# Kernel tuning notes

Hardware: AMD Instinct MI355X
Metric: run time of the kernel (lower is better)

The kernel has to match this reference:

```python
import jax, jax.numpy as jnp
import numpy as np

B, N, D = 4, 1024, 1024
NH = 16
HS = D // NH
HID = 4 * D
EPS = 1e-5

def layernorm(x, w, b):
    mu = jnp.mean(x, axis=-1, keepdims=True)
    var = jnp.mean(jnp.square(x - mu), axis=-1, keepdims=True)
    return (x - mu) * jax.lax.rsqrt(var + EPS) * w + b

def setup_inputs() -> dict:
    key = jax.random.key(0)
    ks = jax.random.split(key, 8)
    s = lambda fan_in: 1.0 / np.sqrt(fan_in)
    return {
        "x": jax.random.normal(ks[0], (B, N, D), jnp.float32),
        "qkv_w": jax.random.uniform(ks[1], (3 * D, D), jnp.float32, -s(D), s(D)),
        "proj_w": jax.random.uniform(ks[2], (D, D), jnp.float32, -s(D), s(D)),
        "proj_b": jax.random.uniform(ks[3], (D,), jnp.float32, -s(D), s(D)),
        "ln1_w": jnp.ones((D,), jnp.float32),
        "ln1_b": jnp.zeros((D,), jnp.float32),
        "fc1_w": jax.random.uniform(ks[4], (HID, D), jnp.float32, -s(D), s(D)),
        "fc1_b": jax.random.uniform(ks[5], (HID,), jnp.float32, -s(D), s(D)),
        "fc2_w": jax.random.uniform(ks[6], (D, HID), jnp.float32, -s(HID), s(HID)),
        "fc2_b": jax.random.uniform(ks[7], (D,), jnp.float32, -s(HID), s(HID)),
        "ln2_w": jnp.ones((D,), jnp.float32),
        "ln2_b": jnp.zeros((D,), jnp.float32),
    }

def attention(x, qkv_w, proj_w, proj_b):
    # x: [b, n, d]; qkv linear (no bias), split into q,k,v per head
    qkv = jnp.einsum('bnd,ed->bne', x, qkv_w)              # [b, n, 3d]
    qkv = qkv.reshape(B, N, 3, NH, HS).transpose(2, 0, 3, 1, 4)  # [3, b, nh, n, hs]
    q, k, v = qkv[0], qkv[1], qkv[2]
    scale = HS ** -0.5
    # mask=False => self.mask == 1, so (mask-1)*LARGE_NUMBER == 0
    att = jax.nn.softmax(scale * jnp.einsum('bhqe,bhke->bhqk', q, k), axis=-1)
    y = jnp.einsum('bhqk,bhke->bhqe', att, v)              # [b, nh, n, hs]
    y = y.transpose(0, 2, 1, 3).reshape(B, N, D)
    return jnp.einsum('bnd,ed->bne', y, proj_w) + proj_b

def mlp(x, fc1_w, fc1_b, fc2_w, fc2_b):
    h = jax.nn.gelu(jnp.einsum('bnd,hd->bnh', x, fc1_w) + fc1_b, approximate=False)
    return jnp.einsum('bnh,dh->bnd', h, fc2_w) + fc2_b

def reference(x, qkv_w, proj_w, proj_b, ln1_w, ln1_b, fc1_w, fc1_b, fc2_w, fc2_b, ln2_w, ln2_b):
    x = x + attention(layernorm(x, ln1_w, ln1_b), qkv_w, proj_w, proj_b)
    x = x + mlp(layernorm(x, ln2_w, ln2_b), fc1_w, fc1_b, fc2_w, fc2_b)
    return x
```

## Files before the change

### kernel.cpp

```cpp
#include <hip/hip_runtime.h>
#include <hip/hip_bf16.h>

typedef __attribute__((ext_vector_type(8))) short short8;
typedef __attribute__((ext_vector_type(8))) unsigned short ushort8;
typedef __attribute__((ext_vector_type(4))) float floatx4;

#define DEV static __device__ __forceinline__

DEV unsigned short f2bf(float f) {
  unsigned int u = __builtin_bit_cast(unsigned int, f);
  u += 0x7fff + ((u >> 16) & 1);
  return (unsigned short)(u >> 16);
}
DEV float bf2f(unsigned short u) {
  return __builtin_bit_cast(float, (unsigned int)u << 16);
}

DEV void gload_lds16(const void* g, void* l) {
  __builtin_amdgcn_global_load_lds(
      (const __attribute__((address_space(1))) unsigned int*)g,
      (__attribute__((address_space(3))) unsigned int*)l, 16, 0, 0);
}

__global__ __launch_bounds__(256) void cvt4_kernel(const float* __restrict__ w0,
                                                   const float* __restrict__ w1,
                                                   const float* __restrict__ w2,
                                                   const float* __restrict__ w3,
                                                   unsigned short* __restrict__ o0,
                                                   unsigned short* __restrict__ o1,
                                                   unsigned short* __restrict__ o2,
                                                   unsigned short* __restrict__ o3) {
  int i = blockIdx.x * 256 + threadIdx.x;
  const float* in; unsigned short* out; int j;
  if (i < 786432)       { in = w0; out = o0; j = i; }
  else if (i < 1048576) { in = w1; out = o1; j = i - 786432; }
  else if (i < 2097152) { in = w2; out = o2; j = i - 1048576; }
  else                  { in = w3; out = o3; j = i - 2097152; }
  float4 v = reinterpret_cast<const float4*>(in)[j];
  ushort4 o;
  o.x = f2bf(v.x); o.y = f2bf(v.y); o.z = f2bf(v.z); o.w = f2bf(v.w);
  reinterpret_cast<ushort4*>(out)[j] = o;
}

__global__ __launch_bounds__(256) void ln_kernel(const float* __restrict__ x,
                                                 const float* __restrict__ w,
                                                 const float* __restrict__ b,
                                                 unsigned short* __restrict__ out) {
  const int row = blockIdx.x;
  const float* xr = x + (size_t)row * 1024;
  float4 v = reinterpret_cast<const float4*>(xr)[threadIdx.x];
  float s  = v.x + v.y + v.z + v.w;
  float ss = v.x*v.x + v.y*v.y + v.z*v.z + v.w*v.w;
  #pragma unroll
  for (int off = 1; off < 64; off <<= 1) {
    s  += __shfl_xor(s, off);
    ss += __shfl_xor(ss, off);
  }
  __shared__ float red[8];
  const int wid = threadIdx.x >> 6, lane = threadIdx.x & 63;
  if (lane == 0) { red[wid] = s; red[4 + wid] = ss; }
  __syncthreads();
  s  = red[0] + red[1] + red[2] + red[3];
  ss = red[4] + red[5] + red[6] + red[7];
  const float mu  = s * (1.0f / 1024.0f);
  const float var = ss * (1.0f / 1024.0f) - mu * mu;
  const float rstd = rsqrtf(var + 1e-5f);
  float4 wv = reinterpret_cast<const float4*>(w)[threadIdx.x];
  float4 bv = reinterpret_cast<const float4*>(b)[threadIdx.x];
  ushort4 o;
  o.x = f2bf((v.x - mu) * rstd * wv.x + bv.x);
  o.y = f2bf((v.y - mu) * rstd * wv.y + bv.y);
  o.z = f2bf((v.z - mu) * rstd * wv.z + bv.z);
  o.w = f2bf((v.w - mu) * rstd * wv.w + bv.w);
  reinterpret_cast<ushort4*>(out)[(size_t)row * 256 + threadIdx.x] = o;
}

template<int EPI>
__global__ __launch_bounds__(512, 2) void gemm256(const unsigned short* __restrict__ A,
                                                  const unsigned short* __restrict__ Bw,
                                                  unsigned short* __restrict__ outb,
                                                  const float* __restrict__ bias,
                                                  int K, int N, int NT) {
  __shared__ unsigned short As[2][256 * 64];
  __shared__ unsigned short Bs[2][256 * 64];
  const int tid = threadIdx.x, lane = tid & 63, wid = tid >> 6;
  const int wr = wid >> 2, wc = wid & 3;
  const int fr = lane & 15, s0 = lane >> 4;

  const int nwg = gridDim.x;
  const int qq = nwg >> 3, rr8 = nwg & 7, xcd = blockIdx.x & 7, lid = blockIdx.x >> 3;
  const int wg = (xcd < rr8 ? xcd * (qq + 1) : rr8 * (qq + 1) + (xcd - rr8) * qq) + lid;
  const int brow = (wg / NT) * 256, bcol = (wg % NT) * 256;

  const unsigned short* ag[4];
  const unsigned short* bg[4];
  #pragma unroll
  for (int L = 0; L < 4; L++) {
    const int idx = L * 512 + tid;
    const int row = idx >> 3;
    const int ss  = ((idx & 7) ^ (row & 7)) * 8;
    ag[L] = A  + (size_t)(brow + row) * K + ss;
    bg[L] = Bw + (size_t)(bcol + row) * K + ss;
  }
  const int ldst = tid * 8;

  #define STG256(kt, buf)                                                     \
    do {                                                                      \
      const int ko = (kt) * 64;                                               \
      gload_lds16(ag[0] + ko, &As[buf][ldst]);                                \
      gload_lds16(ag[1] + ko, &As[buf][4096 + ldst]);                         \
      gload_lds16(ag[2] + ko, &As[buf][8192 + ldst]);                         \
      gload_lds16(ag[3] + ko, &As[buf][12288 + ldst]);                        \
      gload_lds16(bg[0] + ko, &Bs[buf][ldst]);                                \
      gload_lds16(bg[1] + ko, &Bs[buf][4096 + ldst]);                         \
      gload_lds16(bg[2] + ko, &Bs[buf][8192 + ldst]);                         \
      gload_lds16(bg[3] + ko, &Bs[buf][12288 + ldst]);                        \
    } while (0)

  const int xs = fr & 7;
  const int aoff = (wr * 128 + fr) * 64;
  const int boff = (wc * 64 + fr) * 64;
  const int sl0 = ((0 + s0) ^ xs) * 8;
  const int sl1 = ((4 + s0) ^ xs) * 8;

  floatx4 acc[8][4];
  #pragma unroll
  for (int m = 0; m < 8; m++)
    #pragma unroll
    for (int n = 0; n < 4; n++) acc[m][n] = (floatx4){0.f, 0.f, 0.f, 0.f};

  const int NTK = K >> 6;
  STG256(0, 0);

  for (int kt = 0; kt < NTK; ++kt) {
    const int cur = kt & 1;
    if (kt + 1 < NTK) {
      STG256(kt + 1, cur ^ 1);
      asm volatile("s_waitcnt vmcnt(8)" ::: "memory");
    } else {
      asm volatile("s_waitcnt vmcnt(0)" ::: "memory");
    }
    __builtin_amdgcn_s_barrier();

    const unsigned short* Ac = As[cur];
    const unsigned short* Bc = Bs[cur];
    short8 a0[4][2], a1[4][2], b0[2][2], b1[2][2];

    #pragma unroll
    for (int m = 0; m < 4; m++) {
      a0[m][0] = *reinterpret_cast<const short8*>(Ac + aoff + m * 1024 + sl0);
      a0[m][1] = *reinterpret_cast<const short8*>(Ac + aoff + m * 1024 + sl1);
    }
    #pragma unroll
    for (int n = 0; n < 2; n++) {
      b0[n][0] = *reinterpret_cast<const short8*>(Bc + boff + n * 1024 + sl0);
      b0[n][1] = *reinterpret_cast<const short8*>(Bc + boff + n * 1024 + sl1);
    }
    __builtin_amdgcn_s_barrier();
    __builtin_amdgcn_s_setprio(1);
    #pragma unroll
    for (int m = 0; m < 4; m++)
      #pragma unroll
      for (int n = 0; n < 2; n++) {
        acc[m][n] = __builtin_amdgcn_mfma_f32_16x16x32_bf16(a0[m][0], b0[n][0], acc[m][n], 0, 0, 0);
        acc[m][n] = __builtin_amdgcn_mfma_f32_16x16x32_bf16(a0[m][1], b0[n][1], acc[m][n], 0, 0, 0);
      }
    __builtin_amdgcn_s_setprio(0);
    __builtin_amdgcn_s_barrier();

    #pragma unroll
    for (int n = 0; n < 2; n++) {
      b1[n][0] = *reinterpret_cast<const short8*>(Bc + boff + (n + 2) * 1024 + sl0);
      b1[n][1] = *reinterpret_cast<const short8*>(Bc + boff + (n + 2) * 1024 + sl1);
    }
    __builtin_amdgcn_s_barrier();
    __builtin_amdgcn_s_setprio(1);
    #pragma unroll
    for (int m = 0; m < 4; m++)
      #pragma unroll
      for (int n = 0; n < 2; n++) {
        acc[m][n + 2] = __builtin_amdgcn_mfma_f32_16x16x32_bf16(a0[m][0], b1[n][0], acc[m][n + 2], 0, 0, 0);
        acc[m][n + 2] = __builtin_amdgcn_mfma_f32_16x16x32_bf16(a0[m][1], b1[n][1], acc[m][n + 2], 0, 0, 0);
      }
    __builtin_amdgcn_s_setprio(0);
    __builtin_amdgcn_s_barrier();

    #pragma unroll
    for (int m = 0; m < 4; m++) {
      a1[m][0] = *reinterpret_cast<const short8*>(Ac + aoff + (m + 4) * 1024 + sl0);
      a1[m][1] = *reinterpret_cast<const short8*>(Ac + aoff + (m + 4) * 1024 + sl1);
    }
    __builtin_amdgcn_s_barrier();
    __builtin_amdgcn_s_setprio(1);
    #pragma unroll
    for (int m = 0; m < 4; m++)
      #pragma unroll
      for (int n = 0; n < 2; n++) {
        acc[m + 4][n] = __builtin_amdgcn_mfma_f32_16x16x32_bf16(a1[m][0], b0[n][0], acc[m + 4][n], 0, 0, 0);
        acc[m + 4][n] = __builtin_amdgcn_mfma_f32_16x16x32_bf16(a1[m][1], b0[n][1], acc[m + 4][n], 0, 0, 0);
      }
    __builtin_amdgcn_s_setprio(0);
    __builtin_amdgcn_s_barrier();

    __builtin_amdgcn_s_setprio(1);
    #pragma unroll
    for (int m = 0; m < 4; m++)
      #pragma unroll
      for (int n = 0; n < 2; n++) {
        acc[m + 4][n + 2] = __builtin_amdgcn_mfma_f32_16x16x32_bf16(a1[m][0], b1[n][0], acc[m + 4][n + 2], 0, 0, 0);
        acc[m + 4][n + 2] = __builtin_amdgcn_mfma_f32_16x16x32_bf16(a1[m][1], b1[n][1], acc[m + 4][n + 2], 0, 0, 0);
      }
    __builtin_amdgcn_s_setprio(0);
    __builtin_amdgcn_s_barrier();
  }
  #undef STG256

  #pragma unroll
  for (int m = 0; m < 8; m++) {
    #pragma unroll
    for (int n = 0; n < 4; n++) {
      const int col = bcol + wc * 64 + n * 16 + fr;
      #pragma unroll
      for (int r = 0; r < 4; r++) {
        const size_t idx = (size_t)(brow + wr * 128 + m * 16 + s0 * 4 + r) * N + col;
        float v = acc[m][n][r];
        if (EPI == 1) {
          v += bias[col];
          const float u = v * 0.7978845608f * (1.0f + 0.044715f * v * v);
          const float e = __expf(2.0f * u);
          v = v * (e / (e + 1.0f));
        }
        outb[idx] = f2bf(v);
      }
    }
  }
}

__global__ __launch_bounds__(512) void gemm128sk(const unsigned short* __restrict__ A,
                                                 const unsigned short* __restrict__ Bw,
                                                 unsigned short* __restrict__ outb,
                                                 int K, int Ksl, int N, int NT, int ntiles) {
  __shared__ unsigned short As[4][128 * 32];
  __shared__ unsigned short Bs[4][128 * 32];
  const int tid = threadIdx.x, lane = tid & 63, wid = tid >> 6;
  const int wrow = (wid >> 2) * 64, wcol = (wid & 3) * 32;
  const int fr = lane & 15, s0 = lane >> 4;

  const int nwg = gridDim.x;
  const int qq = nwg >> 3, rr8 = nwg & 7, xcd = blockIdx.x & 7, lid = blockIdx.x >> 3;
  const int wg = (xcd < rr8 ? xcd * (qq + 1) : rr8 * (qq + 1) + (xcd - rr8) * qq) + lid;
  const int kslice = wg / ntiles, t = wg % ntiles;
  const int brow = (t / NT) * 128, bcol = (t % NT) * 128;
  const int kofs = kslice * Ksl;

  const int srow = tid >> 2;
  const int sslot = ((tid & 3) ^ ((srow >> 1) & 3)) * 8;
  const unsigned short* ag = A  + (size_t)(brow + srow) * K + kofs + sslot;
  const unsigned short* bg = Bw + (size_t)(bcol + srow) * K + kofs + sslot;
  const int ldst = tid * 8;

  #define STG(kt, buf)                              \
    do {                                            \
      const int ko = (kt) * 32;                     \
      gload_lds16(ag + ko, &As[buf][ldst]);         \
      gload_lds16(bg + ko, &Bs[buf][ldst]);         \
    } while (0)

  const int slr = (s0 ^ ((fr >> 1) & 3)) * 8;

  floatx4 acc[4][2];
  #pragma unroll
  for (int i = 0; i < 4; i++)
    #pragma unroll
    for (int j = 0; j < 2; j++) acc[i][j] = (floatx4){0.f, 0.f, 0.f, 0.f};

  const int NTK = Ksl >> 5;
  STG(0, 0);
  STG(1, 1);
  STG(2, 2);

  for (int kt = 0; kt < NTK; ++kt) {
    const int cur = kt & 3;
    if (kt + 3 < NTK) {
      STG(kt + 3, (kt + 3) & 3);
      asm volatile("s_waitcnt vmcnt(6)" ::: "memory");
    } else if (kt + 2 < NTK) {
      asm volatile("s_waitcnt vmcnt(4)" ::: "memory");
    } else if (kt + 1 < NTK) {
      asm volatile("s_waitcnt vmcnt(2)" ::: "memory");
    } else {
      asm volatile("s_waitcnt vmcnt(0)" ::: "memory");
    }
    __builtin_amdgcn_s_barrier();

    short8 af[4], bf[2];
    #pragma unroll
    for (int i = 0; i < 4; i++)
      af[i] = *reinterpret_cast<const short8*>(&As[cur][(wrow + i * 16 + fr) * 32 + slr]);
    #pragma unroll
    for (int j = 0; j < 2; j++)
      bf[j] = *reinterpret_cast<const short8*>(&Bs[cur][(wcol + j * 16 + fr) * 32 + slr]);
    __builtin_amdgcn_s_setprio(1);
    #pragma unroll
    for (int i = 0; i < 4; i++)
      #pragma unroll
      for (int j = 0; j < 2; j++)
        acc[i][j] = __builtin_amdgcn_mfma_f32_16x16x32_bf16(af[i], bf[j], acc[i][j], 0, 0, 0);
    __builtin_amdgcn_s_setprio(0);
    __builtin_amdgcn_s_barrier();
  }
  #undef STG

  unsigned short* po = outb + (size_t)kslice * ((size_t)ntiles * 16384);
  const int erow = brow + wrow + (s0 << 2);
  const int ecol = bcol + wcol + fr;
  #pragma unroll
  for (int i = 0; i < 4; i++)
    #pragma unroll
    for (int j = 0; j < 2; j++)
      #pragma unroll
      for (int r = 0; r < 4; r++)
        po[(size_t)(erow + i * 16 + r) * N + ecol + j * 16] = f2bf(acc[i][j][r]);
}

__global__ __launch_bounds__(256) void red_ln(const unsigned short* __restrict__ p0,
                                              const unsigned short* __restrict__ p1,
                                              const float* __restrict__ x,
                                              const float* __restrict__ bias,
                                              const float* __restrict__ lw,
                                              const float* __restrict__ lb,
                                              float* __restrict__ x1,
                                              unsigned short* __restrict__ xn) {
  const int row = blockIdx.x, t = threadIdx.x;
  const size_t o4 = (size_t)row * 256 + t;
  ushort4 a = reinterpret_cast<const ushort4*>(p0)[o4];
  ushort4 c = reinterpret_cast<const ushort4*>(p1)[o4];
  float4 xv = reinterpret_cast<const float4*>(x)[o4];
  float4 bv = reinterpret_cast<const float4*>(bias)[t];
  float4 v;
  v.x = bf2f(a.x) + bf2f(c.x) + bv.x + xv.x;
  v.y = bf2f(a.y) + bf2f(c.y) + bv.y + xv.y;
  v.z = bf2f(a.z) + bf2f(c.z) + bv.z + xv.z;
  v.w = bf2f(a.w) + bf2f(c.w) + bv.w + xv.w;
  reinterpret_cast<float4*>(x1)[o4] = v;

  float s  = v.x + v.y + v.z + v.w;
  float ss = v.x*v.x + v.y*v.y + v.z*v.z + v.w*v.w;
  #pragma unroll
  for (int off = 1; off < 64; off <<= 1) {
    s  += __shfl_xor(s, off);
    ss += __shfl_xor(ss, off);
  }
  __shared__ float red[8];
  const int wid = t >> 6, lane = t & 63;
  if (lane == 0) { red[wid] = s; red[4 + wid] = ss; }
  __syncthreads();
  s  = red[0] + red[1] + red[2] + red[3];
  ss = red[4] + red[5] + red[6] + red[7];
  const float mu  = s * (1.0f / 1024.0f);
  const float var = ss * (1.0f / 1024.0f) - mu * mu;
  const float rstd = rsqrtf(var + 1e-5f);
  float4 wv = reinterpret_cast<const float4*>(lw)[t];
  float4 lv = reinterpret_cast<const float4*>(lb)[t];
  ushort4 o;
  o.x = f2bf((v.x - mu) * rstd * wv.x + lv.x);
  o.y = f2bf((v.y - mu) * rstd * wv.y + lv.y);
  o.z = f2bf((v.z - mu) * rstd * wv.z + lv.z);
  o.w = f2bf((v.w - mu) * rstd * wv.w + lv.w);
  reinterpret_cast<ushort4*>(xn)[o4] = o;
}

__global__ __launch_bounds__(256) void red_out(const unsigned short* __restrict__ p0,
                                               const unsigned short* __restrict__ p1,
                                               const float* __restrict__ x1,
                                               const float* __restrict__ bias,
                                               float* __restrict__ out) {
  const size_t i4 = (size_t)blockIdx.x * 256 + threadIdx.x;
  const int c4 = (int)(i4 & 255);
  ushort4 a = reinterpret_cast<const ushort4*>(p0)[i4];
  ushort4 c = reinterpret_cast<const ushort4*>(p1)[i4];
  float4 xv = reinterpret_cast<const float4*>(x1)[i4];
  float4 bv = reinterpret_cast<const float4*>(bias)[c4];
  float4 v;
  v.x = bf2f(a.x) + bf2f(c.x) + bv.x + xv.x;
  v.y = bf2f(a.y) + bf2f(c.y) + bv.y + xv.y;
  v.z = bf2f(a.z) + bf2f(c.z) + bv.z + xv.z;
  v.w = bf2f(a.w) + bf2f(c.w) + bv.w + xv.w;
  reinterpret_cast<float4*>(out)[i4] = v;
}

__global__ __launch_bounds__(256) void vtrans_kernel(const unsigned short* __restrict__ qkv,
                                                     unsigned short* __restrict__ vt) {
  __shared__ unsigned short T[64][66];
  const int nt = blockIdx.x, bh = blockIdx.y;
  const int b = bh >> 4, h = bh & 15;
  const unsigned short* src = qkv + (size_t)b * 1024 * 3072 + 2048 + h * 64;
  const int r = threadIdx.x >> 3, s = threadIdx.x & 7;
  ushort8 a0 = *reinterpret_cast<const ushort8*>(src + (size_t)(nt * 64 + r) * 3072 + s * 8);
  ushort8 a1 = *reinterpret_cast<const ushort8*>(src + (size_t)(nt * 64 + r + 32) * 3072 + s * 8);
  #pragma unroll
  for (int j = 0; j < 8; j++) {
    T[r][s * 8 + j]      = a0[j];
    T[r + 32][s * 8 + j] = a1[j];
  }
  __syncthreads();
  ushort8 o0, o1;
  #pragma unroll
  for (int j = 0; j < 8; j++) {
    o0[j] = T[s * 8 + j][r];
    o1[j] = T[s * 8 + j][r + 32];
  }
  unsigned short* dst = vt + (size_t)bh * 64 * 1024 + nt * 64 + s * 8;
  *reinterpret_cast<ushort8*>(dst + (size_t)r * 1024)        = o0;
  *reinterpret_cast<ushort8*>(dst + (size_t)(r + 32) * 1024) = o1;
}

__global__ __launch_bounds__(256) void attn_kernel(const unsigned short* __restrict__ qkv,
                                                   const unsigned short* __restrict__ vt,
                                                   unsigned short* __restrict__ y) {
  __shared__ unsigned short Ks[2][64 * 64];
  __shared__ unsigned short Vs[2][64 * 64];
  __shared__ unsigned short Ps[4][16 * 64];

  const int tid = threadIdx.x;
  const int lane = tid & 63;
  const int w = tid >> 6;
  const int wg = (blockIdx.x & 7) * 128 + (blockIdx.x >> 3);
  const int bh = wg >> 4, qt = wg & 15;
  const int b = bh >> 4, h = bh & 15;
  const int fr = lane & 15, s0 = lane >> 4;
  const int fk = s0 * 8;
  const int sw = fr & 7;
  const size_t RS = 3072;

  const unsigned short* qbase = qkv + (size_t)b * 1024 * RS + h * 64;
  const unsigned short* kbase = qbase + 1024;
  const unsigned short* vbase = vt + (size_t)bh * 64 * 1024;

  short8 aq[2];
  {
    const unsigned short* qrow = qbase + (size_t)(qt * 64 + w * 16 + fr) * RS;
    aq[0] = *reinterpret_cast<const short8*>(qrow + fk);
    aq[1] = *reinterpret_cast<const short8*>(qrow + 32 + fk);
  }

  float m_run[4], l_run[4];
  floatx4 accy[4];
  #pragma unroll
  for (int r = 0; r < 4; r++) { m_run[r] = -1e30f; l_run[r] = 0.f; }
  #pragma unroll
  for (int d = 0; d < 4; d++) accy[d] = (floatx4){0.f, 0.f, 0.f, 0.f};

  const int krow0 = tid >> 3, kslot = tid & 7;
  const int gslot = (kslot ^ (krow0 & 7)) * 8;
  const unsigned short* kg0 = kbase + (size_t)krow0 * RS + gslot;
  const unsigned short* kg1 = kbase + (size_t)(krow0 + 32) * RS + gslot;
  const unsigned short* vg0 = vbase + (size_t)krow0 * 1024 + gslot;
  const unsigned short* vg1 = vbase + (size_t)(krow0 + 32) * 1024 + gslot;

  #define STAGE(t, buf)                                          \
    do {                                                         \
      const size_t ko = (size_t)(t) * 64 * RS;                   \
      const size_t vo = (size_t)(t) * 64;                        \
      gload_lds16(kg0 + ko, &Ks[buf][tid * 8]);                  \
      gload_lds16(kg1 + ko, &Ks[buf][(256 + tid) * 8]);          \
      gload_lds16(vg0 + vo, &Vs[buf][tid * 8]);                  \
      gload_lds16(vg1 + vo, &Vs[buf][(256 + tid) * 8]);          \
    } while (0)

  STAGE(0, 0);
  int cur = 0;

  for (int kt = 0; kt < 16; ++kt) {
    if (kt < 15) {
      STAGE(kt + 1, cur ^ 1);
      asm volatile("s_waitcnt vmcnt(4)" ::: "memory");
    } else {
      asm volatile("s_waitcnt vmcnt(0)" ::: "memory");
    }
    __builtin_amdgcn_s_barrier();

    const unsigned short* Kt = Ks[cur];
    const unsigned short* Vc = Vs[cur];

    floatx4 sfr[4];
    #pragma unroll
    for (int f = 0; f < 4; ++f) {
      floatx4 s = (floatx4){0.f, 0.f, 0.f, 0.f};
      const unsigned short* krow = Kt + (f * 16 + fr) * 64;
      short8 kb0 = *reinterpret_cast<const short8*>(krow + (((s0)     ^ sw) << 3));
      short8 kb1 = *reinterpret_cast<const short8*>(krow + (((s0 + 4) ^ sw) << 3));
      s = __builtin_amdgcn_mfma_f32_16x16x32_bf16(aq[0], kb0, s, 0, 0, 0);
      s = __builtin_amdgcn_mfma_f32_16x16x32_bf16(aq[1], kb1, s, 0, 0, 0);
      sfr[f] = s * 0.125f;
    }

    #pragma unroll
    for (int r = 0; r < 4; r++) {
      float mv = fmaxf(fmaxf(sfr[0][r], sfr[1][r]), fmaxf(sfr[2][r], sfr[3][r]));
      #pragma unroll
      for (int m = 1; m < 16; m <<= 1) mv = fmaxf(mv, __shfl_xor(mv, m));
      const float mn = fmaxf(m_run[r], mv);
      const float alpha = __expf(m_run[r] - mn);
      m_run[r] = mn;
      const int q = s0 * 4 + r;
      const int qx = (q & 7) << 3;
      float ps = 0.f;
      #pragma unroll
      for (int f = 0; f < 4; f++) {
        float p = __expf(sfr[f][r] - mn);
        ps += p;
        Ps[w][q * 64 + ((f * 16 + fr) ^ qx)] = f2bf(p);
      }
      #pragma unroll
      for (int m = 1; m < 16; m <<= 1) ps += __shfl_xor(ps, m);
      l_run[r] = l_run[r] * alpha + ps;
      #pragma unroll
      for (int d = 0; d < 4; d++) accy[d][r] *= alpha;
    }

    #pragma unroll
    for (int ks = 0; ks < 2; ++ks) {
      const int sA = ((ks * 4 + s0) ^ sw) << 3;
      short8 ap = *reinterpret_cast<const short8*>(&Ps[w][fr * 64 + sA]);
      #pragma unroll
      for (int j = 0; j < 4; ++j) {
        short8 vb = *reinterpret_cast<const short8*>(Vc + (j * 16 + fr) * 64 + sA);
        accy[j] = __builtin_amdgcn_mfma_f32_16x16x32_bf16(ap, vb, accy[j], 0, 0, 0);
      }
    }
    __builtin_amdgcn_s_barrier();
    cur ^= 1;
  }
  #undef STAGE

  #pragma unroll
  for (int r = 0; r < 4; r++) {
    const float inv = 1.0f / l_run[r];
    const size_t grow =
        (size_t)(b * 1024 + qt * 64 + w * 16 + s0 * 4 + r) * 1024 + h * 64;
    #pragma unroll
    for (int d = 0; d < 4; ++d)
      y[grow + d * 16 + fr] = f2bf(accy[d][r] * inv);
  }
}

extern "C" void kernel_launch(void* const* d_in, const int* in_sizes, int n_in,
                              void* d_out, int out_size, void* d_ws, size_t ws_size,
                              hipStream_t stream) {
  const float* x      = (const float*)d_in[0];
  const float* qkv_w  = (const float*)d_in[1];
  const float* proj_w = (const float*)d_in[2];
  const float* proj_b = (const float*)d_in[3];
  const float* ln1_w  = (const float*)d_in[4];
  const float* ln1_b  = (const float*)d_in[5];
  const float* fc1_w  = (const float*)d_in[6];
  const float* fc1_b  = (const float*)d_in[7];
  const float* fc2_w  = (const float*)d_in[8];
  const float* fc2_b  = (const float*)d_in[9];
  const float* ln2_w  = (const float*)d_in[10];
  const float* ln2_b  = (const float*)d_in[11];
  float* out = (float*)d_out;

  char* ws = (char*)d_ws;
  unsigned short* qkvw16  = (unsigned short*)(ws + 0);
  unsigned short* projw16 = (unsigned short*)(ws + 6291456);
  unsigned short* fc1w16  = (unsigned short*)(ws + 8388608);
  unsigned short* fc2w16  = (unsigned short*)(ws + 16777216);
  float*          x1      = (float*)(ws + 25165824);
  unsigned short* vt      = (unsigned short*)(ws + 25165824);
  unsigned short* xn      = (unsigned short*)(ws + 41943040);
  unsigned short* big     = (unsigned short*)(ws + 50331648);
  unsigned short* pp      = big;
  unsigned short* fp      = (unsigned short*)(ws + 0);

  cvt4_kernel<<<12288, 256, 0, stream>>>(qkv_w, proj_w, fc1_w, fc2_w,
                                         qkvw16, projw16, fc1w16, fc2w16);

  ln_kernel<<<4096, 256, 0, stream>>>(x, ln1_w, ln1_b, xn);
  gemm256<0><<<192, 512, 0, stream>>>(xn, qkvw16, big, nullptr, 1024, 3072, 12);
  vtrans_kernel<<<dim3(16, 64), 256, 0, stream>>>(big, vt);
  attn_kernel<<<1024, 256, 0, stream>>>(big, vt, xn);
  gemm128sk<<<512, 512, 0, stream>>>(xn, projw16, pp, 1024, 512, 1024, 8, 256);
  red_ln<<<4096, 256, 0, stream>>>(pp, pp + 4194304, x, proj_b, ln2_w, ln2_b, x1, xn);
  gemm256<1><<<256, 512, 0, stream>>>(xn, fc1w16, big, fc1_b, 1024, 4096, 16);
  gemm128sk<<<512, 512, 0, stream>>>(big, fc2w16, fp, 4096, 2048, 1024, 8, 256);
  red_out<<<4096, 256, 0, stream>>>(fp, fp + 4194304, x1, fc2_b, out);
}
```

Measured before the change: 252.7 us.

## Read K/V directly from global memory in attention, add lazy rescaling and exp2 softmax

The attention kernel drops the double-buffered LDS staging of K and V tiles and its barriers. Each wave now loads K and V fragments straight from global memory, relying on the caches, and raises wave priority around the MFMA blocks. Softmax switches to exp2 with the log2e factor folded into the scale. The running max and accumulator rescale now happen only when some row's max grows by more than a threshold. This removes barriers and LDS traffic, but adds redundant global loads across the four waves and accepts bounded growth in the unnormalised accumulator.

```diff
diff --git a/kernel.cpp b/kernel.cpp
--- a/kernel.cpp
+++ b/kernel.cpp
@@ -418,8 +418,6 @@
 __global__ __launch_bounds__(256) void attn_kernel(const unsigned short* __restrict__ qkv,
                                                    const unsigned short* __restrict__ vt,
                                                    unsigned short* __restrict__ y) {
-  __shared__ unsigned short Ks[2][64 * 64];
-  __shared__ unsigned short Vs[2][64 * 64];
   __shared__ unsigned short Ps[4][16 * 64];
 
   const int tid = threadIdx.x;
@@ -429,8 +427,6 @@
   const int bh = wg >> 4, qt = wg & 15;
   const int b = bh >> 4, h = bh & 15;
   const int fr = lane & 15, s0 = lane >> 4;
-  const int fk = s0 * 8;
-  const int sw = fr & 7;
   const size_t RS = 3072;
 
   const unsigned short* qbase = qkv + (size_t)b * 1024 * RS + h * 64;
@@ -440,10 +436,11 @@
   short8 aq[2];
   {
     const unsigned short* qrow = qbase + (size_t)(qt * 64 + w * 16 + fr) * RS;
-    aq[0] = *reinterpret_cast<const short8*>(qrow + fk);
-    aq[1] = *reinterpret_cast<const short8*>(qrow + 32 + fk);
-  }
-
+    aq[0] = *reinterpret_cast<const short8*>(qrow + s0 * 8);
+    aq[1] = *reinterpret_cast<const short8*>(qrow + 32 + s0 * 8);
+  }
+
+  const float SC = 0.125f * 1.44269504089f;
   float m_run[4], l_run[4];
   floatx4 accy[4];
   #pragma unroll
@@ -451,97 +448,86 @@
   #pragma unroll
   for (int d = 0; d < 4; d++) accy[d] = (floatx4){0.f, 0.f, 0.f, 0.f};
 
-  const int krow0 = tid >> 3, kslot = tid & 7;
-  const int gslot = (kslot ^ (krow0 & 7)) * 8;
-  const unsigned short* kg0 = kbase + (size_t)krow0 * RS + gslot;
-  const unsigned short* kg1 = kbase + (size_t)(krow0 + 32) * RS + gslot;
-  const unsigned short* vg0 = vbase + (size_t)krow0 * 1024 + gslot;
-  const unsigned short* vg1 = vbase + (size_t)(krow0 + 32) * 1024 + gslot;
-
-  #define STAGE(t, buf)                                          \
-    do {                                                         \
-      const size_t ko = (size_t)(t) * 64 * RS;                   \
-      const size_t vo = (size_t)(t) * 64;                        \
-      gload_lds16(kg0 + ko, &Ks[buf][tid * 8]);                  \
-      gload_lds16(kg1 + ko, &Ks[buf][(256 + tid) * 8]);          \
-      gload_lds16(vg0 + vo, &Vs[buf][tid * 8]);                  \
-      gload_lds16(vg1 + vo, &Vs[buf][(256 + tid) * 8]);          \
-    } while (0)
-
-  STAGE(0, 0);
-  int cur = 0;
+  const int sw = fr & 7;
 
   for (int kt = 0; kt < 16; ++kt) {
-    if (kt < 15) {
-      STAGE(kt + 1, cur ^ 1);
-      asm volatile("s_waitcnt vmcnt(4)" ::: "memory");
-    } else {
-      asm volatile("s_waitcnt vmcnt(0)" ::: "memory");
-    }
-    __builtin_amdgcn_s_barrier();
-
-    const unsigned short* Kt = Ks[cur];
-    const unsigned short* Vc = Vs[cur];
+    const int kvoff = kt * 64;
 
     floatx4 sfr[4];
+    __builtin_amdgcn_s_setprio(1);
     #pragma unroll
     for (int f = 0; f < 4; ++f) {
+      const unsigned short* kg = kbase + (size_t)(kvoff + f * 16 + fr) * RS + s0 * 8;
+      short8 kb0 = *reinterpret_cast<const short8*>(kg);
+      short8 kb1 = *reinterpret_cast<const short8*>(kg + 32);
       floatx4 s = (floatx4){0.f, 0.f, 0.f, 0.f};
-      const unsigned short* krow = Kt + (f * 16 + fr) * 64;
-      short8 kb0 = *reinterpret_cast<const short8*>(krow + (((s0)     ^ sw) << 3));
-      short8 kb1 = *reinterpret_cast<const short8*>(krow + (((s0 + 4) ^ sw) << 3));
       s = __builtin_amdgcn_mfma_f32_16x16x32_bf16(aq[0], kb0, s, 0, 0, 0);
       s = __builtin_amdgcn_mfma_f32_16x16x32_bf16(aq[1], kb1, s, 0, 0, 0);
-      sfr[f] = s * 0.125f;
-    }
-
+      sfr[f] = s * SC;
+    }
+    __builtin_amdgcn_s_setprio(0);
+
+    float mv[4];
     #pragma unroll
     for (int r = 0; r < 4; r++) {
-      float mv = fmaxf(fmaxf(sfr[0][r], sfr[1][r]), fmaxf(sfr[2][r], sfr[3][r]));
-      #pragma unroll
-      for (int m = 1; m < 16; m <<= 1) mv = fmaxf(mv, __shfl_xor(mv, m));
-      const float mn = fmaxf(m_run[r], mv);
-      const float alpha = __expf(m_run[r] - mn);
-      m_run[r] = mn;
+      float t = fmaxf(fmaxf(sfr[0][r], sfr[1][r]), fmaxf(sfr[2][r], sfr[3][r]));
+      #pragma unroll
+      for (int m = 1; m < 16; m <<= 1) t = fmaxf(t, __shfl_xor(t, m));
+      mv[r] = t;
+    }
+    bool grow = (mv[0] > m_run[0] + 8.f) || (mv[1] > m_run[1] + 8.f) ||
+                (mv[2] > m_run[2] + 8.f) || (mv[3] > m_run[3] + 8.f);
+    if (__any(grow)) {
+      #pragma unroll
+      for (int r = 0; r < 4; r++) {
+        const float mn = fmaxf(m_run[r], mv[r]);
+        const float alpha = exp2f(m_run[r] - mn);
+        m_run[r] = mn;
+        l_run[r] *= alpha;
+        #pragma unroll
+        for (int d = 0; d < 4; d++) accy[d][r] *= alpha;
+      }
+    }
+
+    #pragma unroll
+    for (int r = 0; r < 4; r++) {
       const int q = s0 * 4 + r;
       const int qx = (q & 7) << 3;
       float ps = 0.f;
       #pragma unroll
       for (int f = 0; f < 4; f++) {
-        float p = __expf(sfr[f][r] - mn);
+        float p = exp2f(sfr[f][r] - m_run[r]);
         ps += p;
         Ps[w][q * 64 + ((f * 16 + fr) ^ qx)] = f2bf(p);
       }
       #pragma unroll
       for (int m = 1; m < 16; m <<= 1) ps += __shfl_xor(ps, m);
-      l_run[r] = l_run[r] * alpha + ps;
-      #pragma unroll
-      for (int d = 0; d < 4; d++) accy[d][r] *= alpha;
-    }
-
+      l_run[r] += ps;
+    }
+
+    __builtin_amdgcn_s_setprio(1);
     #pragma unroll
     for (int ks = 0; ks < 2; ++ks) {
       const int sA = ((ks * 4 + s0) ^ sw) << 3;
       short8 ap = *reinterpret_cast<const short8*>(&Ps[w][fr * 64 + sA]);
+      const int kvc = kvoff + (ks * 4 + s0) * 8;
       #pragma unroll
       for (int j = 0; j < 4; ++j) {
-        short8 vb = *reinterpret_cast<const short8*>(Vc + (j * 16 + fr) * 64 + sA);
+        short8 vb = *reinterpret_cast<const short8*>(vbase + (size_t)(j * 16 + fr) * 1024 + kvc);
         accy[j] = __builtin_amdgcn_mfma_f32_16x16x32_bf16(ap, vb, accy[j], 0, 0, 0);
       }
     }
-    __builtin_amdgcn_s_barrier();
-    cur ^= 1;
-  }
-  #undef STAGE
+    __builtin_amdgcn_s_setprio(0);
+  }
 
   #pragma unroll
   for (int r = 0; r < 4; r++) {
     const float inv = 1.0f / l_run[r];
-    const size_t grow =
+    const size_t grow2 =
         (size_t)(b * 1024 + qt * 64 + w * 16 + s0 * 4 + r) * 1024 + h * 64;
     #pragma unroll
     for (int d = 0; d < 4; ++d)
-      y[grow + d * 16 + fr] = f2bf(accy[d][r] * inv);
+      y[grow2 + d * 16 + fr] = f2bf(accy[d][r] * inv);
   }
 }
 
```

New measurement: 314.4 us. 1.24x slower.
